# Kernel tuning notes

Hardware: AMD Instinct MI355X
Metric: run time of the kernel (lower is better)

## Reference

```python
import jax, jax.numpy as jnp
import numpy as np

B, N, C, C_OUT, E = 8, 1024, 256, 256, 16384


def setup_inputs() -> dict:
    key = jax.random.key(0)
    k1, k2, k3 = jax.random.split(key, 3)
    x = jax.random.normal(k1, (B, N, C), dtype=jnp.float32)
    edge_index = jax.random.randint(k2, (2, E, B), 0, N)  # [2, E, B], values in [0, N)
    W = jax.random.normal(k3, (C_OUT, C), dtype=jnp.float32) * 0.02  # torch Linear weight [out, in]
    b = jnp.zeros((C_OUT,), dtype=jnp.float32)
    return {"x": x, "edge_index": edge_index, "W": W, "b": b}


def reference(x, edge_index, W, b):
    Bs, Nn, Cc = x.shape
    BN = Bs * Nn
    # Vectorized version of the per-batch python loop: offset each graph's
    # node indices into the big block-diagonal adjacency.
    offs = jnp.arange(Bs, dtype=edge_index.dtype) * Nn          # [B]
    src = (edge_index[0] + offs[None, :]).reshape(-1)           # [E*B]
    dst = (edge_index[1] + offs[None, :]).reshape(-1)           # [E*B]
    adj = jnp.zeros((BN, BN), dtype=x.dtype).at[src, dst].set(1.0)
    adj = adj + jnp.eye(BN, dtype=x.dtype)                      # self loops (adds on top, as in torch code)
    D = adj.sum(axis=1)                                         # [BN]
    d_inv_sqrt = jnp.where(D > 0, jax.lax.rsqrt(D), 0.0)        # pow(-0.5) with inf -> 0
    adj_n = d_inv_sqrt[:, None] * adj * d_inv_sqrt[None, :]     # D^-1/2 A D^-1/2
    h = adj_n @ x.reshape(BN, Cc)                               # [BN, C]
    out = h @ W.T + b                                           # Linear
    return out.reshape(Bs, Nn, -1)
```

## Files before the change

kernel.cpp:

```cpp
#include <hip/hip_runtime.h>
#include <stdint.h>

#define B_   8
#define N_   1024
#define C_   256
#define E_   16384
#define BN_  (B_ * N_)
#define NW_  (N_ / 32)
#define LIST_CAP 96

typedef __attribute__((ext_vector_type(8))) short bf16x8;
typedef __attribute__((ext_vector_type(4))) float f32x4;

static __device__ __forceinline__ short f32_to_bf16(float f) {
  uint32_t u = __float_as_uint(f);
  uint32_t r = (u + 0x7fffu + ((u >> 16) & 1u)) >> 16;
  return (short)r;
}
static __device__ __forceinline__ float bf16_to_f32(short s) {
  return __uint_as_float(((uint32_t)(uint16_t)s) << 16);
}

__global__ __launch_bounds__(256) void scatter_edges(
    const int* __restrict__ ei, uint32_t* __restrict__ mask) {
  int t = blockIdx.x * 256 + threadIdx.x;
  if (t >= E_ * B_) return;
  int b   = t & (B_ - 1);
  int src = ei[t];
  int dst = ei[E_ * B_ + t];
  int row = b * N_ + src;
  atomicOr(&mask[row * NW_ + (dst >> 5)], 1u << (dst & 31));
}

__global__ __launch_bounds__(256) void gemm_bf16x3(
    const float* __restrict__ X, const float* __restrict__ W,
    const uint32_t* __restrict__ mask, float* __restrict__ Z) {
  __shared__ __attribute__((aligned(16))) short Bh[32][64][8];
  __shared__ __attribute__((aligned(16))) short Bl[32][64][8];
  __shared__ int   dpart[4][64];
  __shared__ float dinv_s[64];

  int t   = threadIdx.x;
  int id  = blockIdx.x;
  int loc = id >> 3;
  int mt  = (id & 7) * 16 + (loc >> 2);
  int m0  = mt * 64;
  int n0  = (loc & 3) * 64;

  {
    int row = t & 63, part = t >> 6;
    const uint4* mp =
        (const uint4*)&mask[(size_t)(m0 + row) * NW_ + part * 8];
    uint4 a = mp[0], b = mp[1];
    dpart[part][row] = __popc(a.x) + __popc(a.y) + __popc(a.z) + __popc(a.w) +
                       __popc(b.x) + __popc(b.y) + __popc(b.z) + __popc(b.w);
  }

#pragma unroll
  for (int i = 0; i < 8; i++) {
    int row = t & 63;
    int ch  = (t >> 6) * 8 + i;
    const float* wr = &W[(size_t)(n0 + row) * C_ + ch * 8];
    float w8[8];
    *(float4*)&w8[0] = *(const float4*)&wr[0];
    *(float4*)&w8[4] = *(const float4*)&wr[4];
    bf16x8 wh, wl;
#pragma unroll
    for (int j = 0; j < 8; j++) {
      short h = f32_to_bf16(w8[j]);
      wh[j] = h;
      wl[j] = f32_to_bf16(w8[j] - bf16_to_f32(h));
    }
    *(bf16x8*)&Bh[ch][row][0] = wh;
    *(bf16x8*)&Bl[ch][row][0] = wl;
  }
  __syncthreads();

  if (t < 64) {
    int d = dpart[0][t] + dpart[1][t] + dpart[2][t] + dpart[3][t] + 1;
    dinv_s[t] = rsqrtf((float)d);
  }

  int wv = t >> 6;
  int ln = t & 63;
  int lm = ln & 15;
  int qd = ln >> 4;

  const float* xr = &X[(size_t)(m0 + 16 * wv + lm) * C_ + qd * 8];

  f32x4 acc[4];
#pragma unroll
  for (int i = 0; i < 4; i++) acc[i] = (f32x4){0.f, 0.f, 0.f, 0.f};

#pragma unroll
  for (int k0 = 0; k0 < C_; k0 += 32) {
    float xv[8];
    *(float4*)&xv[0] = *(const float4*)&xr[k0];
    *(float4*)&xv[4] = *(const float4*)&xr[k0 + 4];
    bf16x8 ah, al;
#pragma unroll
    for (int j = 0; j < 8; j++) {
      short h = f32_to_bf16(xv[j]);
      ah[j] = h;
      al[j] = f32_to_bf16(xv[j] - bf16_to_f32(h));
    }
    int cq = (k0 >> 3) + qd;
#pragma unroll
    for (int nt = 0; nt < 4; nt++) {
      bf16x8 bh = *(const bf16x8*)&Bh[cq][nt * 16 + lm][0];
      bf16x8 bl = *(const bf16x8*)&Bl[cq][nt * 16 + lm][0];
      acc[nt] = __builtin_amdgcn_mfma_f32_16x16x32_bf16(ah, bh, acc[nt], 0, 0, 0);
      acc[nt] = __builtin_amdgcn_mfma_f32_16x16x32_bf16(ah, bl, acc[nt], 0, 0, 0);
      acc[nt] = __builtin_amdgcn_mfma_f32_16x16x32_bf16(al, bh, acc[nt], 0, 0, 0);
    }
  }
  __syncthreads();

  float di[4];
#pragma unroll
  for (int r = 0; r < 4; r++) di[r] = dinv_s[16 * wv + qd * 4 + r];
#pragma unroll
  for (int nt = 0; nt < 4; nt++) {
#pragma unroll
    for (int r = 0; r < 4; r++) {
      int m = m0 + 16 * wv + qd * 4 + r;
      int n = n0 + nt * 16 + lm;
      Z[(size_t)m * C_ + n] = di[r] * acc[nt][r];
    }
  }
}

__global__ __launch_bounds__(256) void aggregate(
    const uint32_t* __restrict__ mask, const float* __restrict__ Z,
    const float* __restrict__ bias, float* __restrict__ out) {
  __shared__ uint16_t lists[4][LIST_CAP];

  int blk   = blockIdx.x;
  int batch = blk & 7;
  int group = blk >> 3;
  int wv    = threadIdx.x >> 6;
  int ln    = threadIdx.x & 63;
  int loc   = group * 4 + wv;
  int node  = batch * N_ + loc;
  int c4    = ln * 4;

  uint32_t bits = (ln < NW_) ? mask[(size_t)node * NW_ + ln] : 0u;
  int cnt = __popc(bits);
  int pfx = cnt;
#pragma unroll
  for (int off = 1; off < 64; off <<= 1) {
    int v = __shfl_up(pfx, off);
    if (ln >= off) pfx += v;
  }
  int total = __shfl(pfx, 63);
  pfx -= cnt;
  uint16_t* lst = lists[wv];
  int o = pfx, jb = ln * 32;
  while (bits) {
    int j = __ffs(bits) - 1;
    bits &= bits - 1;
    lst[o++] = (uint16_t)(jb + j);
  }
  if (ln == 0) {
    int dd = total;
    while (dd & 3) lst[dd++] = 0;
  }

  const float* zb = Z + (size_t)batch * N_ * C_;
  float4 acc = *(const float4*)&zb[(size_t)loc * C_ + c4];

  for (int k = 0; k < total; k += 4) {
    ushort4 n4 = *(const ushort4*)&lst[k];
    float4 z0 = *(const float4*)&zb[(size_t)n4.x * C_ + c4];
    float4 z1 = *(const float4*)&zb[(size_t)n4.y * C_ + c4];
    float4 z2 = *(const float4*)&zb[(size_t)n4.z * C_ + c4];
    float4 z3 = *(const float4*)&zb[(size_t)n4.w * C_ + c4];
    float w1 = (k + 1 < total) ? 1.f : 0.f;
    float w2 = (k + 2 < total) ? 1.f : 0.f;
    float w3 = (k + 3 < total) ? 1.f : 0.f;
    acc.x += z0.x; acc.y += z0.y; acc.z += z0.z; acc.w += z0.w;
    acc.x += w1 * z1.x; acc.y += w1 * z1.y; acc.z += w1 * z1.z; acc.w += w1 * z1.w;
    acc.x += w2 * z2.x; acc.y += w2 * z2.y; acc.z += w2 * z2.z; acc.w += w2 * z2.w;
    acc.x += w3 * z3.x; acc.y += w3 * z3.y; acc.z += w3 * z3.z; acc.w += w3 * z3.w;
  }

  float di = rsqrtf((float)(total + 1));
  float4 bb = *(const float4*)&bias[c4];
  float4 o4;
  o4.x = di * acc.x + bb.x;
  o4.y = di * acc.y + bb.y;
  o4.z = di * acc.z + bb.z;
  o4.w = di * acc.w + bb.w;
  *(float4*)&out[(size_t)node * C_ + c4] = o4;
}

extern "C" void kernel_launch(void* const* d_in, const int* in_sizes, int n_in,
                              void* d_out, int out_size, void* d_ws,
                              size_t ws_size, hipStream_t stream) {
  const float* x    = (const float*)d_in[0];
  const int*   ei   = (const int*)d_in[1];
  const float* W    = (const float*)d_in[2];
  const float* bias = (const float*)d_in[3];
  float*       out  = (float*)d_out;

  char* ws = (char*)d_ws;
  uint32_t* mask = (uint32_t*)(ws + 0x000000);
  float*    Z    = (float*)   (ws + 0x100000);

  hipMemsetAsync(mask, 0, (size_t)BN_ * NW_ * 4, stream);

  scatter_edges<<<(E_ * B_) / 256, 256, 0, stream>>>(ei, mask);
  gemm_bf16x3<<<512, 256, 0, stream>>>(x, W, mask, Z);
  aggregate<<<BN_ / 4, 256, 0, stream>>>(mask, Z, bias, out);
}
```

Baseline: 95.46 us.

## Fuse mask clear, edge scatter and GEMM into one cooperative kernel

Replaces the memset, the scatter kernel and the GEMM kernel with a single cooperative launch of 512 blocks. Inside it, the mask is zeroed, edges are scattered with atomicOr, and then the GEMM runs, with grid-wide syncs between phases. This removes two launches and the memset, and adds the cost of two grid barriers plus a cooperative launch, which requires all 512 blocks to be resident at once.

After: 312.0 us. +226.8%, slower.

```diff
diff --git a/kernel.cpp b/kernel.cpp
--- a/kernel.cpp
+++ b/kernel.cpp
@@ -1,4 +1,5 @@
 #include <hip/hip_runtime.h>
+#include <hip/hip_cooperative_groups.h>
 #include <stdint.h>
 
 #define B_   8
@@ -21,27 +22,36 @@
   return __uint_as_float(((uint32_t)(uint16_t)s) << 16);
 }
 
-__global__ __launch_bounds__(256) void scatter_edges(
-    const int* __restrict__ ei, uint32_t* __restrict__ mask) {
-  int t = blockIdx.x * 256 + threadIdx.x;
-  if (t >= E_ * B_) return;
-  int b   = t & (B_ - 1);
-  int src = ei[t];
-  int dst = ei[E_ * B_ + t];
-  int row = b * N_ + src;
-  atomicOr(&mask[row * NW_ + (dst >> 5)], 1u << (dst & 31));
-}
-
-__global__ __launch_bounds__(256) void gemm_bf16x3(
-    const float* __restrict__ X, const float* __restrict__ W,
-    const uint32_t* __restrict__ mask, float* __restrict__ Z) {
+__global__ __launch_bounds__(256) void fused_pre(
+    const float* __restrict__ X, const int* __restrict__ ei,
+    const float* __restrict__ W, uint32_t* __restrict__ mask,
+    float* __restrict__ Z) {
   __shared__ __attribute__((aligned(16))) short Bh[32][64][8];
   __shared__ __attribute__((aligned(16))) short Bl[32][64][8];
   __shared__ int   dpart[4][64];
   __shared__ float dinv_s[64];
 
-  int t   = threadIdx.x;
-  int id  = blockIdx.x;
+  cooperative_groups::grid_group gg = cooperative_groups::this_grid();
+
+  int t    = threadIdx.x;
+  int id   = blockIdx.x;
+  int gtid = id * 256 + t;
+
+  ((uint2*)mask)[gtid] = make_uint2(0u, 0u);
+  __threadfence();
+  gg.sync();
+  __threadfence();
+
+  {
+    int b   = gtid & (B_ - 1);
+    int src = ei[gtid];
+    int dst = ei[E_ * B_ + gtid];
+    atomicOr(&mask[(size_t)(b * N_ + src) * NW_ + (dst >> 5)], 1u << (dst & 31));
+  }
+  __threadfence();
+  gg.sync();
+  __threadfence();
+
   int loc = id >> 3;
   int mt  = (id & 7) * 16 + (loc >> 2);
   int m0  = mt * 64;
@@ -207,9 +217,8 @@
   uint32_t* mask = (uint32_t*)(ws + 0x000000);
   float*    Z    = (float*)   (ws + 0x100000);
 
-  hipMemsetAsync(mask, 0, (size_t)BN_ * NW_ * 4, stream);
-
-  scatter_edges<<<(E_ * B_) / 256, 256, 0, stream>>>(ei, mask);
-  gemm_bf16x3<<<512, 256, 0, stream>>>(x, W, mask, Z);
+  void* args[] = {(void*)&x, (void*)&ei, (void*)&W, (void*)&mask, (void*)&Z};
+  hipLaunchCooperativeKernel((void*)fused_pre, dim3(512), dim3(256), args, 0,
+                             stream);
   aggregate<<<BN_ / 4, 256, 0, stream>>>(mask, Z, bias, out);
 }
```
